# Optimization experiments

Measured on AMD Instinct MI355X. Metric: run time of the kernel, lower is better.

## Reference

```python
import jax, jax.numpy as jnp
import numpy as np

IN_FEATS = 16
OUT_FEATS = 16
EDGE_FEATS = 16
N_NODES = 50000
N_EDGES = 800000


def setup_inputs() -> dict:
    key = jax.random.key(0)
    k = jax.random.split(key, 7)
    feat = jax.random.normal(k[0], (N_NODES, IN_FEATS), dtype=jnp.float32)
    efeat = jax.random.normal(k[1], (N_EDGES, EDGE_FEATS), dtype=jnp.float32)
    # edge_nn = Linear(EDGE_FEATS, IN_FEATS*OUT_FEATS)
    We = jax.random.normal(k[2], (EDGE_FEATS, IN_FEATS * OUT_FEATS), dtype=jnp.float32) * 0.1
    be = jax.random.normal(k[3], (IN_FEATS * OUT_FEATS,), dtype=jnp.float32) * 0.1
    bias = jax.random.normal(k[4], (OUT_FEATS,), dtype=jnp.float32) * 0.1
    src = jax.random.randint(k[5], (N_EDGES,), 0, N_NODES, dtype=jnp.int64 if jax.config.jax_enable_x64 else jnp.int32)
    dst = jnp.sort(jax.random.randint(k[6], (N_EDGES,), 0, N_NODES, dtype=jnp.int64 if jax.config.jax_enable_x64 else jnp.int32))
    return {"feat": feat, "efeat": efeat, "We": We, "be": be, "bias": bias,
            "src": src, "dst": dst, "num_nodes": N_NODES}


def reference(feat, efeat, We, be, bias, src, dst, num_nodes):
    # edge-conditioned weights: [E, in, out]
    w = (efeat @ We + be).reshape(-1, IN_FEATS, OUT_FEATS)
    # gather source features and per-edge matvec: sum_i h_src[e,i] * w[e,i,o]
    m = jnp.einsum('ei,eio->eo', feat[src], w)  # [E, out]
    # segment-sum aggregation to destination nodes ('sum' reducer)
    neigh = jax.ops.segment_sum(m, dst, num_segments=num_nodes)  # [N, out]
    # residual (Identity since in_feats == out_feats) + bias
    return neigh + feat + bias
```

## Files before the change

kernel.cpp:

```cpp
#include <hip/hip_runtime.h>

typedef __attribute__((ext_vector_type(2))) _Float16 half2v;
typedef __attribute__((ext_vector_type(8))) _Float16 half8v;
typedef __attribute__((ext_vector_type(4))) float f32x4;

#define NBLK 2048
#define WT (NBLK * 4)
#define WP_ELEMS (9 * 4 * 16 * 8)
#define RP_OFF 16384
#define MS_OFF (16384 + 262144)

__global__ __launch_bounds__(256) void setup_kernel(
    const float* __restrict__ We, const float* __restrict__ be,
    const int* __restrict__ dst,
    unsigned short* __restrict__ wp, int* __restrict__ rp,
    int E, int N) {
  int idx = blockIdx.x * 256 + threadIdx.x;
  if (idx < WP_ELEMS) {
    int j = idx & 7, n = (idx >> 3) & 15, gg = (idx >> 7) & 3, t = idx >> 9;
    float v = 0.f;
    if (t < 8) {
      int c = (gg >> 1) * 8 + t;
      int i = (gg & 1) * 8 + j;
      v = We[c * 256 + i * 16 + n];
    } else if (gg < 2) {
      v = be[(gg * 8 + j) * 16 + n];
    }
    _Float16 hv = (_Float16)v;
    wp[idx] = __builtin_bit_cast(unsigned short, hv);
  }
  if (idx <= N) {
    int lo = 0, hi = E;
    while (lo < hi) {
      int mid = (lo + hi) >> 1;
      if (dst[mid] < idx) lo = mid + 1; else hi = mid;
    }
    rp[idx] = lo;
  }
}

__device__ __forceinline__ void cvt_mask_write(char* bufb, int lane,
                                               float4 ve, float4 vh, bool vld) {
  if (!vld) { ve = make_float4(0.f, 0.f, 0.f, 0.f); vh = ve; }
  half2v e0 = half2v{(_Float16)ve.x, (_Float16)ve.y};
  half2v e1 = half2v{(_Float16)ve.z, (_Float16)ve.w};
  half2v h0 = half2v{(_Float16)vh.x, (_Float16)vh.y};
  half2v h1 = half2v{(_Float16)vh.z, (_Float16)vh.w};
  uint2 ew, hw;
  ew.x = __builtin_bit_cast(unsigned, e0); ew.y = __builtin_bit_cast(unsigned, e1);
  hw.x = __builtin_bit_cast(unsigned, h0); hw.y = __builtin_bit_cast(unsigned, h1);
  int el = lane >> 2, q = lane & 3;
  *reinterpret_cast<uint2*>(bufb + el * 48 + q * 8) = ew;
  *reinterpret_cast<uint2*>(bufb + 768 + el * 48 + q * 8) = hw;
}

__device__ __forceinline__ void compute_store(
    unsigned short* __restrict__ ms, int tile, const char* bufb,
    int g, int m, int lane, const half8v* Bf) {
  int p = g >> 1, hh = g & 1;
  half8v efr = *reinterpret_cast<const half8v*>(bufb + m * 48 + p * 16);
  half8v hfr = *reinterpret_cast<const half8v*>(bufb + 768 + m * 48 + hh * 16);
  half2v ef2[4], h2[4];
#pragma unroll
  for (int j = 0; j < 4; ++j) {
    ef2[j] = half2v{efr[2 * j], efr[2 * j + 1]};
    h2[j]  = half2v{hfr[2 * j], hfr[2 * j + 1]};
  }
  f32x4 accA = {0.f, 0.f, 0.f, 0.f};
  f32x4 accB = {0.f, 0.f, 0.f, 0.f};
#pragma unroll
  for (int t = 0; t < 8; ++t) {
    _Float16 ev = ef2[t >> 1][t & 1];
    half2v evb = half2v{ev, ev};
    half2v a0 = evb * h2[0], a1 = evb * h2[1], a2 = evb * h2[2], a3 = evb * h2[3];
    half8v A;
    A[0] = a0[0]; A[1] = a0[1]; A[2] = a1[0]; A[3] = a1[1];
    A[4] = a2[0]; A[5] = a2[1]; A[6] = a3[0]; A[7] = a3[1];
    if (t & 1)
      accB = __builtin_amdgcn_mfma_f32_16x16x32_f16(A, Bf[t], accB, 0, 0, 0);
    else
      accA = __builtin_amdgcn_mfma_f32_16x16x32_f16(A, Bf[t], accA, 0, 0, 0);
  }
  {
    half2v z = half2v{(_Float16)0.f, (_Float16)0.f};
    half2v b0 = (g < 2) ? h2[0] : z, b1 = (g < 2) ? h2[1] : z;
    half2v b2 = (g < 2) ? h2[2] : z, b3 = (g < 2) ? h2[3] : z;
    half8v A;
    A[0] = b0[0]; A[1] = b0[1]; A[2] = b1[0]; A[3] = b1[1];
    A[4] = b2[0]; A[5] = b2[1]; A[6] = b3[0]; A[7] = b3[1];
    accB = __builtin_amdgcn_mfma_f32_16x16x32_f16(A, Bf[8], accB, 0, 0, 0);
  }
  half2v lo = half2v{(_Float16)(accA[0] + accB[0]), (_Float16)(accA[1] + accB[1])};
  half2v hi = half2v{(_Float16)(accA[2] + accB[2]), (_Float16)(accA[3] + accB[3])};
  uint2 w;
  w.x = __builtin_bit_cast(unsigned, lo);
  w.y = __builtin_bit_cast(unsigned, hi);
  *reinterpret_cast<uint2*>(ms + (size_t)tile * 256 + lane * 4) = w;
}

__global__ __launch_bounds__(256) void edge_gemm_kernel(
    const float* __restrict__ feat, const float* __restrict__ efeat,
    const int* __restrict__ src, const unsigned short* __restrict__ wp,
    unsigned short* __restrict__ ms, int E) {
  __shared__ __align__(16) char lds[4][2][1536];
  int wid = threadIdx.x >> 6;
  int lane = threadIdx.x & 63;
  int g = lane >> 4, m = lane & 15;
  int el = lane >> 2, q = lane & 3;

  int ntiles = (E + 15) >> 4;
  int wave = blockIdx.x * 4 + wid;
  if (wave >= ntiles) return;

  half8v Bf[9];
#pragma unroll
  for (int t = 0; t < 9; ++t)
    Bf[t] = *reinterpret_cast<const half8v*>(wp + (unsigned)(t * 64 + lane) * 8);

  int t = wave;
  {
    int eg = min(t * 16 + el, E - 1);
    int s  = src[eg];
    float4 ve = *reinterpret_cast<const float4*>(efeat + (size_t)eg * 16 + q * 4);
    float4 vh = *reinterpret_cast<const float4*>(feat + (size_t)s * 16 + q * 4);
    cvt_mask_write(&lds[wid][0][0], lane, ve, vh, (t * 16 + el) < E);
  }
  int t1 = t + WT;
  int s1 = (t1 < ntiles) ? src[min(t1 * 16 + el, E - 1)] : 0;
  int b = 0;

  while (t1 < ntiles) {
    int t2 = t1 + WT;
    int s2 = src[min(min(t2, ntiles - 1) * 16 + el, E - 1)];
    int eg1 = min(t1 * 16 + el, E - 1);
    float4 ve = *reinterpret_cast<const float4*>(efeat + (size_t)eg1 * 16 + q * 4);
    float4 vh = *reinterpret_cast<const float4*>(feat + (size_t)s1 * 16 + q * 4);
    __builtin_amdgcn_sched_barrier(0);

    compute_store(ms, t, &lds[wid][b][0], g, m, lane, Bf);

    asm volatile("s_waitcnt vmcnt(1)" ::: "memory");
    __builtin_amdgcn_sched_barrier(0);
    cvt_mask_write(&lds[wid][b ^ 1][0], lane, ve, vh, (t1 * 16 + el) < E);

    s1 = s2;
    t = t1; t1 = t2; b ^= 1;
  }
  compute_store(ms, t, &lds[wid][b][0], g, m, lane, Bf);
}

__device__ __forceinline__ float ms_at(const unsigned short* ms, int e, int c) {
  unsigned short u = ms[((e >> 4) << 8) + (((e >> 2) & 3) << 6) + (c << 2) + (e & 3)];
  return (float)__builtin_bit_cast(_Float16, u);
}

__global__ __launch_bounds__(256) void segsum_kernel(
    const float* __restrict__ feat, const float* __restrict__ bias,
    const unsigned short* __restrict__ ms, const int* __restrict__ rp,
    float* __restrict__ out, int N) {
  int n = blockIdx.x * 16 + (threadIdx.x >> 4);
  int c = threadIdx.x & 15;
  if (n >= N) return;
  int lo = rp[n], hi = rp[n + 1];
  float sum = 0.f;
  int e = lo;
  while (e < hi && (e & 3)) { sum += ms_at(ms, e, c); ++e; }
  while (e + 4 <= hi) {
    const uint2 v = *reinterpret_cast<const uint2*>(
        ms + ((e >> 4) << 8) + (((e >> 2) & 3) << 6) + (c << 2));
    half2v x = __builtin_bit_cast(half2v, v.x);
    half2v y = __builtin_bit_cast(half2v, v.y);
    sum += (float)x[0] + (float)x[1] + (float)y[0] + (float)y[1];
    e += 4;
  }
  while (e < hi) { sum += ms_at(ms, e, c); ++e; }
  out[n * 16 + c] = sum + feat[n * 16 + c] + bias[c];
}

extern "C" void kernel_launch(void* const* d_in, const int* in_sizes, int n_in,
                              void* d_out, int out_size, void* d_ws, size_t ws_size,
                              hipStream_t stream) {
  const float* feat  = (const float*)d_in[0];
  const float* efeat = (const float*)d_in[1];
  const float* We    = (const float*)d_in[2];
  const float* be    = (const float*)d_in[3];
  const float* bias  = (const float*)d_in[4];
  const int*   src   = (const int*)d_in[5];
  const int*   dst   = (const int*)d_in[6];
  float* out = (float*)d_out;

  int E = in_sizes[5];
  int N = out_size / 16;

  unsigned short* wp = (unsigned short*)d_ws;
  int* rp = (int*)((char*)d_ws + RP_OFF);
  unsigned short* ms = (unsigned short*)((char*)d_ws + MS_OFF);

  int setup_items = (N + 1) > WP_ELEMS ? (N + 1) : WP_ELEMS;
  setup_kernel<<<(setup_items + 255) / 256, 256, 0, stream>>>(We, be, dst, wp, rp, E, N);

  int ntiles = (E + 15) / 16;
  int blocksA = min(NBLK, (ntiles + 3) / 4);
  edge_gemm_kernel<<<blocksA, 256, 0, stream>>>(feat, efeat, src, wp, ms, E);

  int blocksB = (N + 15) / 16;
  segsum_kernel<<<blocksB, 256, 0, stream>>>(feat, bias, ms, rp, out, N);
}
```

Baseline: 42.67 us.

## Prefetch two 32-edge groups ahead with fp16 feature copy in edge GEMM

The setup kernel now also writes an fp16 copy of the node features, so the edge kernel gathers half as many bytes per source node. The edge kernel handles 32-edge groups, uses half as many blocks, and keeps two register banks of loads in flight with a deeper vmcnt wait. Loads for a group issue two iterations before its compute, which is meant to hide gather latency better. The cost is more registers and LDS per wave, an extra feature-conversion pass, and a larger workspace.

```diff
diff --git a/kernel.cpp b/kernel.cpp
--- a/kernel.cpp
+++ b/kernel.cpp
@@ -2,19 +2,20 @@
 
 typedef __attribute__((ext_vector_type(2))) _Float16 half2v;
 typedef __attribute__((ext_vector_type(8))) _Float16 half8v;
+typedef __attribute__((ext_vector_type(8))) unsigned short ushort8v;
 typedef __attribute__((ext_vector_type(4))) float f32x4;
 
-#define NBLK 2048
-#define WT (NBLK * 4)
+#define NBLK 1024
 #define WP_ELEMS (9 * 4 * 16 * 8)
 #define RP_OFF 16384
-#define MS_OFF (16384 + 262144)
+#define F16_OFF (16384 + 262144)
+#define MS_OFF (F16_OFF + 2097152)
 
 __global__ __launch_bounds__(256) void setup_kernel(
     const float* __restrict__ We, const float* __restrict__ be,
-    const int* __restrict__ dst,
+    const float* __restrict__ feat, const int* __restrict__ dst,
     unsigned short* __restrict__ wp, int* __restrict__ rp,
-    int E, int N) {
+    unsigned short* __restrict__ f16, int E, int N) {
   int idx = blockIdx.x * 256 + threadIdx.x;
   if (idx < WP_ELEMS) {
     int j = idx & 7, n = (idx >> 3) & 15, gg = (idx >> 7) & 3, t = idx >> 9;
@@ -37,116 +38,161 @@
     }
     rp[idx] = lo;
   }
-}
-
-__device__ __forceinline__ void cvt_mask_write(char* bufb, int lane,
-                                               float4 ve, float4 vh, bool vld) {
-  if (!vld) { ve = make_float4(0.f, 0.f, 0.f, 0.f); vh = ve; }
-  half2v e0 = half2v{(_Float16)ve.x, (_Float16)ve.y};
-  half2v e1 = half2v{(_Float16)ve.z, (_Float16)ve.w};
-  half2v h0 = half2v{(_Float16)vh.x, (_Float16)vh.y};
-  half2v h1 = half2v{(_Float16)vh.z, (_Float16)vh.w};
-  uint2 ew, hw;
-  ew.x = __builtin_bit_cast(unsigned, e0); ew.y = __builtin_bit_cast(unsigned, e1);
-  hw.x = __builtin_bit_cast(unsigned, h0); hw.y = __builtin_bit_cast(unsigned, h1);
-  int el = lane >> 2, q = lane & 3;
-  *reinterpret_cast<uint2*>(bufb + el * 48 + q * 8) = ew;
-  *reinterpret_cast<uint2*>(bufb + 768 + el * 48 + q * 8) = hw;
-}
-
-__device__ __forceinline__ void compute_store(
-    unsigned short* __restrict__ ms, int tile, const char* bufb,
-    int g, int m, int lane, const half8v* Bf) {
+  if (idx * 4 < N * 16) {
+    float4 v = *reinterpret_cast<const float4*>(feat + idx * 4);
+    half2v a{(_Float16)v.x, (_Float16)v.y};
+    half2v b{(_Float16)v.z, (_Float16)v.w};
+    uint2 w;
+    w.x = __builtin_bit_cast(unsigned, a);
+    w.y = __builtin_bit_cast(unsigned, b);
+    *reinterpret_cast<uint2*>(f16 + idx * 4) = w;
+  }
+}
+
+struct Bank { float4 ea, eb; ushort8v h; };
+
+__device__ __forceinline__ void issue_grp(
+    Bank& bk, int ni, int n4, int& ss, int E,
+    const float4* __restrict__ ef4, const ushort8v* __restrict__ f16v,
+    const int* __restrict__ src, int eE, int qE, int eH, int qH) {
+  int b0 = ni * 32;
+  bk.ea = ef4[(unsigned)min(b0 + eE, E - 1) * 4 + qE];
+  bk.eb = ef4[(unsigned)min(b0 + 16 + eE, E - 1) * 4 + qE];
+  bk.h  = f16v[(unsigned)ss * 2 + qH];
+  ss = src[min(n4 * 32 + eH, E - 1)];
+}
+
+__device__ __forceinline__ void stage_grp(
+    char* __restrict__ buf, const Bank& bk, int ni, int E,
+    int eE, int qE, int eH, int qH) {
+  half2v x0{(_Float16)bk.ea.x, (_Float16)bk.ea.y};
+  half2v x1{(_Float16)bk.ea.z, (_Float16)bk.ea.w};
+  half2v y0{(_Float16)bk.eb.x, (_Float16)bk.eb.y};
+  half2v y1{(_Float16)bk.eb.z, (_Float16)bk.eb.w};
+  uint2 w0, w1;
+  w0.x = __builtin_bit_cast(unsigned, x0); w0.y = __builtin_bit_cast(unsigned, x1);
+  w1.x = __builtin_bit_cast(unsigned, y0); w1.y = __builtin_bit_cast(unsigned, y1);
+  if ((ni * 32 + eE) >= E)      { w0.x = 0; w0.y = 0; }
+  if ((ni * 32 + 16 + eE) >= E) { w1.x = 0; w1.y = 0; }
+  *reinterpret_cast<uint2*>(buf + eE * 48 + qE * 8) = w0;
+  *reinterpret_cast<uint2*>(buf + (16 + eE) * 48 + qE * 8) = w1;
+  ushort8v hv = bk.h;
+  if ((ni * 32 + eH) >= E) hv = (ushort8v){0, 0, 0, 0, 0, 0, 0, 0};
+  *reinterpret_cast<ushort8v*>(buf + 1536 + eH * 48 + qH * 16) = hv;
+}
+
+__device__ __forceinline__ void compute_st(
+    unsigned short* __restrict__ ms, const char* __restrict__ buf,
+    int ni, int E, int g, int m, int lane, const half8v* Bf) {
   int p = g >> 1, hh = g & 1;
-  half8v efr = *reinterpret_cast<const half8v*>(bufb + m * 48 + p * 16);
-  half8v hfr = *reinterpret_cast<const half8v*>(bufb + 768 + m * 48 + hh * 16);
-  half2v ef2[4], h2[4];
-#pragma unroll
-  for (int j = 0; j < 4; ++j) {
-    ef2[j] = half2v{efr[2 * j], efr[2 * j + 1]};
-    h2[j]  = half2v{hfr[2 * j], hfr[2 * j + 1]};
-  }
-  f32x4 accA = {0.f, 0.f, 0.f, 0.f};
-  f32x4 accB = {0.f, 0.f, 0.f, 0.f};
-#pragma unroll
-  for (int t = 0; t < 8; ++t) {
-    _Float16 ev = ef2[t >> 1][t & 1];
-    half2v evb = half2v{ev, ev};
-    half2v a0 = evb * h2[0], a1 = evb * h2[1], a2 = evb * h2[2], a3 = evb * h2[3];
-    half8v A;
-    A[0] = a0[0]; A[1] = a0[1]; A[2] = a1[0]; A[3] = a1[1];
-    A[4] = a2[0]; A[5] = a2[1]; A[6] = a3[0]; A[7] = a3[1];
-    if (t & 1)
-      accB = __builtin_amdgcn_mfma_f32_16x16x32_f16(A, Bf[t], accB, 0, 0, 0);
-    else
-      accA = __builtin_amdgcn_mfma_f32_16x16x32_f16(A, Bf[t], accA, 0, 0, 0);
-  }
-  {
-    half2v z = half2v{(_Float16)0.f, (_Float16)0.f};
-    half2v b0 = (g < 2) ? h2[0] : z, b1 = (g < 2) ? h2[1] : z;
-    half2v b2 = (g < 2) ? h2[2] : z, b3 = (g < 2) ? h2[3] : z;
-    half8v A;
-    A[0] = b0[0]; A[1] = b0[1]; A[2] = b1[0]; A[3] = b1[1];
-    A[4] = b2[0]; A[5] = b2[1]; A[6] = b3[0]; A[7] = b3[1];
-    accB = __builtin_amdgcn_mfma_f32_16x16x32_f16(A, Bf[8], accB, 0, 0, 0);
-  }
-  half2v lo = half2v{(_Float16)(accA[0] + accB[0]), (_Float16)(accA[1] + accB[1])};
-  half2v hi = half2v{(_Float16)(accA[2] + accB[2]), (_Float16)(accA[3] + accB[3])};
-  uint2 w;
-  w.x = __builtin_bit_cast(unsigned, lo);
-  w.y = __builtin_bit_cast(unsigned, hi);
-  *reinterpret_cast<uint2*>(ms + (size_t)tile * 256 + lane * 4) = w;
+#pragma unroll
+  for (int tt = 0; tt < 2; ++tt) {
+    if ((ni * 32 + tt * 16) >= E) break;
+    half8v efr = *reinterpret_cast<const half8v*>(buf + (tt * 16 + m) * 48 + p * 16);
+    half8v hfr = *reinterpret_cast<const half8v*>(buf + 1536 + (tt * 16 + m) * 48 + hh * 16);
+    half2v ef2[4], h2[4];
+#pragma unroll
+    for (int j = 0; j < 4; ++j) {
+      ef2[j] = half2v{efr[2 * j], efr[2 * j + 1]};
+      h2[j]  = half2v{hfr[2 * j], hfr[2 * j + 1]};
+    }
+    f32x4 accA = {0.f, 0.f, 0.f, 0.f};
+    f32x4 accB = {0.f, 0.f, 0.f, 0.f};
+#pragma unroll
+    for (int t = 0; t < 8; ++t) {
+      _Float16 ev = ef2[t >> 1][t & 1];
+      half2v evb = half2v{ev, ev};
+      half2v a0 = evb * h2[0], a1 = evb * h2[1], a2 = evb * h2[2], a3 = evb * h2[3];
+      half8v A;
+      A[0] = a0[0]; A[1] = a0[1]; A[2] = a1[0]; A[3] = a1[1];
+      A[4] = a2[0]; A[5] = a2[1]; A[6] = a3[0]; A[7] = a3[1];
+      if (t & 1)
+        accB = __builtin_amdgcn_mfma_f32_16x16x32_f16(A, Bf[t], accB, 0, 0, 0);
+      else
+        accA = __builtin_amdgcn_mfma_f32_16x16x32_f16(A, Bf[t], accA, 0, 0, 0);
+    }
+    {
+      half2v z{(_Float16)0.f, (_Float16)0.f};
+      half2v b0 = (g < 2) ? h2[0] : z, b1 = (g < 2) ? h2[1] : z;
+      half2v b2 = (g < 2) ? h2[2] : z, b3 = (g < 2) ? h2[3] : z;
+      half8v A;
+      A[0] = b0[0]; A[1] = b0[1]; A[2] = b1[0]; A[3] = b1[1];
+      A[4] = b2[0]; A[5] = b2[1]; A[6] = b3[0]; A[7] = b3[1];
+      accB = __builtin_amdgcn_mfma_f32_16x16x32_f16(A, Bf[8], accB, 0, 0, 0);
+    }
+    half2v lo{(_Float16)(accA[0] + accB[0]), (_Float16)(accA[1] + accB[1])};
+    half2v hi{(_Float16)(accA[2] + accB[2]), (_Float16)(accA[3] + accB[3])};
+    uint2 w;
+    w.x = __builtin_bit_cast(unsigned, lo);
+    w.y = __builtin_bit_cast(unsigned, hi);
+    *reinterpret_cast<uint2*>(ms + (size_t)(2 * ni + tt) * 256 + lane * 4) = w;
+  }
 }
 
 __global__ __launch_bounds__(256) void edge_gemm_kernel(
-    const float* __restrict__ feat, const float* __restrict__ efeat,
-    const int* __restrict__ src, const unsigned short* __restrict__ wp,
+    const float* __restrict__ efeat, const int* __restrict__ src,
+    const unsigned short* __restrict__ wp, const unsigned short* __restrict__ f16,
     unsigned short* __restrict__ ms, int E) {
-  __shared__ __align__(16) char lds[4][2][1536];
-  int wid = threadIdx.x >> 6;
-  int lane = threadIdx.x & 63;
+  __shared__ __align__(16) char lds[4][2][3072];
+  int wid = threadIdx.x >> 6, lane = threadIdx.x & 63;
   int g = lane >> 4, m = lane & 15;
-  int el = lane >> 2, q = lane & 3;
-
-  int ntiles = (E + 15) >> 4;
-  int wave = blockIdx.x * 4 + wid;
-  if (wave >= ntiles) return;
+  int eE = lane >> 2, qE = lane & 3, eH = lane >> 1, qH = lane & 1;
+
+  int nst = (E + 31) >> 5;
+  int CW = gridDim.x * 4;
+  int n = blockIdx.x * 4 + wid;
+  if (n >= nst) return;
 
   half8v Bf[9];
 #pragma unroll
   for (int t = 0; t < 9; ++t)
     Bf[t] = *reinterpret_cast<const half8v*>(wp + (unsigned)(t * 64 + lane) * 8);
 
-  int t = wave;
+  const float4* ef4 = reinterpret_cast<const float4*>(efeat);
+  const ushort8v* f16v = reinterpret_cast<const ushort8v*>(f16);
+  char* buf0 = &lds[wid][0][0];
+  char* buf1 = &lds[wid][1][0];
+
+  int n1 = n + CW, n2 = n1 + CW, n3 = n2 + CW;
+  int CW2 = 2 * CW;
+  Bank P, Q;
+  int ssA, ssB;
+
   {
-    int eg = min(t * 16 + el, E - 1);
-    int s  = src[eg];
-    float4 ve = *reinterpret_cast<const float4*>(efeat + (size_t)eg * 16 + q * 4);
-    float4 vh = *reinterpret_cast<const float4*>(feat + (size_t)s * 16 + q * 4);
-    cvt_mask_write(&lds[wid][0][0], lane, ve, vh, (t * 16 + el) < E);
-  }
-  int t1 = t + WT;
-  int s1 = (t1 < ntiles) ? src[min(t1 * 16 + el, E - 1)] : 0;
-  int b = 0;
-
-  while (t1 < ntiles) {
-    int t2 = t1 + WT;
-    int s2 = src[min(min(t2, ntiles - 1) * 16 + el, E - 1)];
-    int eg1 = min(t1 * 16 + el, E - 1);
-    float4 ve = *reinterpret_cast<const float4*>(efeat + (size_t)eg1 * 16 + q * 4);
-    float4 vh = *reinterpret_cast<const float4*>(feat + (size_t)s1 * 16 + q * 4);
-    __builtin_amdgcn_sched_barrier(0);
-
-    compute_store(ms, t, &lds[wid][b][0], g, m, lane, Bf);
-
-    asm volatile("s_waitcnt vmcnt(1)" ::: "memory");
-    __builtin_amdgcn_sched_barrier(0);
-    cvt_mask_write(&lds[wid][b ^ 1][0], lane, ve, vh, (t1 * 16 + el) < E);
-
-    s1 = s2;
-    t = t1; t1 = t2; b ^= 1;
-  }
-  compute_store(ms, t, &lds[wid][b][0], g, m, lane, Bf);
+    int ss0 = src[min(n * 32 + eH, E - 1)];
+    Q.ea = ef4[(unsigned)min(n * 32 + eE, E - 1) * 4 + qE];
+    Q.eb = ef4[(unsigned)min(n * 32 + 16 + eE, E - 1) * 4 + qE];
+    Q.h  = f16v[(unsigned)ss0 * 2 + qH];
+    ssA  = src[min(n2 * 32 + eH, E - 1)];
+    int ss1 = src[min(n1 * 32 + eH, E - 1)];
+    stage_grp(buf0, Q, n, E, eE, qE, eH, qH);
+    P.ea = ef4[(unsigned)min(n1 * 32 + eE, E - 1) * 4 + qE];
+    P.eb = ef4[(unsigned)min(n1 * 32 + 16 + eE, E - 1) * 4 + qE];
+    P.h  = f16v[(unsigned)ss1 * 2 + qH];
+    ssB  = src[min(n3 * 32 + eH, E - 1)];
+  }
+
+  while (true) {
+    issue_grp(Q, n2, n2 + CW2, ssA, E, ef4, f16v, src, eE, qE, eH, qH);
+    __builtin_amdgcn_sched_barrier(0);
+    compute_st(ms, buf0, n, E, g, m, lane, Bf);
+    __builtin_amdgcn_sched_barrier(0);
+    if (n1 >= nst) return;
+    asm volatile("s_waitcnt vmcnt(6)" ::: "memory");
+    __builtin_amdgcn_sched_barrier(0);
+    stage_grp(buf1, P, n1, E, eE, qE, eH, qH);
+
+    issue_grp(P, n3, n3 + CW2, ssB, E, ef4, f16v, src, eE, qE, eH, qH);
+    __builtin_amdgcn_sched_barrier(0);
+    compute_st(ms, buf1, n1, E, g, m, lane, Bf);
+    __builtin_amdgcn_sched_barrier(0);
+    if (n2 >= nst) return;
+    asm volatile("s_waitcnt vmcnt(6)" ::: "memory");
+    __builtin_amdgcn_sched_barrier(0);
+    stage_grp(buf0, Q, n2, E, eE, qE, eH, qH);
+
+    n += CW2; n1 += CW2; n2 += CW2; n3 += CW2;
+  }
 }
 
 __device__ __forceinline__ float ms_at(const unsigned short* ms, int e, int c) {
@@ -192,16 +238,20 @@
   int E = in_sizes[5];
   int N = out_size / 16;
 
-  unsigned short* wp = (unsigned short*)d_ws;
-  int* rp = (int*)((char*)d_ws + RP_OFF);
-  unsigned short* ms = (unsigned short*)((char*)d_ws + MS_OFF);
-
-  int setup_items = (N + 1) > WP_ELEMS ? (N + 1) : WP_ELEMS;
-  setup_kernel<<<(setup_items + 255) / 256, 256, 0, stream>>>(We, be, dst, wp, rp, E, N);
-
-  int ntiles = (E + 15) / 16;
-  int blocksA = min(NBLK, (ntiles + 3) / 4);
-  edge_gemm_kernel<<<blocksA, 256, 0, stream>>>(feat, efeat, src, wp, ms, E);
+  unsigned short* wp  = (unsigned short*)d_ws;
+  int* rp             = (int*)((char*)d_ws + RP_OFF);
+  unsigned short* f16 = (unsigned short*)((char*)d_ws + F16_OFF);
+  unsigned short* ms  = (unsigned short*)((char*)d_ws + MS_OFF);
+
+  int sitems = WP_ELEMS;
+  if (N + 1 > sitems) sitems = N + 1;
+  if (N * 4 > sitems) sitems = N * 4;
+  setup_kernel<<<(sitems + 255) / 256, 256, 0, stream>>>(We, be, feat, dst,
+                                                         wp, rp, f16, E, N);
+
+  int nst = (E + 31) / 32;
+  int blocksA = min(NBLK, (nst + 3) / 4);
+  edge_gemm_kernel<<<blocksA, 256, 0, stream>>>(efeat, src, wp, f16, ms, E);
 
   int blocksB = (N + 15) / 16;
   segsum_kernel<<<blocksB, 256, 0, stream>>>(feat, bias, ms, rp, out, N);
```

After: 41.08 us (median of 2 runs). 3.7% less time.
